# Kernel optimization log

Measured on AMD Instinct MI355X. Metric: run time of the kernel, lower is better.

The kernel has to match this reference:

```python
import jax, jax.numpy as jnp
import numpy as np

N, NS, D, HID = 8192, 512, 1024, 1024  # nodes, num_edges, f_dim, mlp hidden (max(f_dim,128))


def layernorm(x, g, b, eps=1e-5):
    m = x.mean(-1, keepdims=True)
    v = x.var(-1, keepdims=True)
    return (x - m) / jnp.sqrt(v + eps) * g + b


def mask_topk(a, kk):
    # keep only the top-kk entries of each row (vectorized version of mask_attn)
    _, idx = jax.lax.top_k(a, kk)
    rows = jnp.arange(a.shape[0])[:, None]
    mask = jnp.zeros(a.shape, a.dtype).at[rows, idx].set(1.0)
    return a * mask


def setup_inputs() -> dict:
    key = jax.random.key(0)
    ks = jax.random.split(key, 16)
    xavier = lambda k, i, o: jax.random.uniform(k, (i, o), jnp.float32, -1.0, 1.0) * np.sqrt(6.0 / (i + o))
    return {
        "inputs": jax.random.normal(ks[0], (N, D), jnp.float32),
        "noise": jax.random.normal(ks[1], (NS, D), jnp.float32),
        "edges_mu": jax.random.normal(ks[2], (1, D), jnp.float32),
        "edges_logsigma": xavier(ks[3], 1, D),
        "Wq": xavier(ks[4], D, D), "bq": jnp.zeros((D,), jnp.float32),
        "Wk": xavier(ks[5], D, D), "bk": jnp.zeros((D,), jnp.float32),
        "Wv": xavier(ks[6], D, D), "bv": jnp.zeros((D,), jnp.float32),
        "W1": xavier(ks[7], 2 * D, HID), "b1": jnp.zeros((HID,), jnp.float32),
        "W2": xavier(ks[8], HID, D), "b2": jnp.zeros((D,), jnp.float32),
        "g_in": jnp.ones((D,), jnp.float32), "b_in": jnp.zeros((D,), jnp.float32),
        "g_e": jnp.ones((D,), jnp.float32), "b_e": jnp.zeros((D,), jnp.float32),
        "k_n": 64,
        "k_e": 8,
    }


def reference(inputs, noise, edges_mu, edges_logsigma, Wq, bq, Wk, bk, Wv, bv,
              W1, b1, W2, b2, g_in, b_in, g_e, b_e, k_n, k_e):
    n, d = inputs.shape
    scale = d ** -0.5
    eps = 1e-8
    x = layernorm(inputs, g_in, b_in)                       # norm_input
    k = jax.nn.relu(x @ Wk + bk)                            # [N, D]
    v = jax.nn.relu(x @ Wv + bv)                            # [N, D]
    edges = edges_mu + jnp.exp(edges_logsigma) * noise      # [NS, D]
    # single iteration (iters=1)
    edges = layernorm(edges, g_e, b_e)                      # norm_edgs
    q = jax.nn.relu(edges @ Wq + bq)                        # [NS, D]
    dots = jnp.einsum('ni,mi->nm', q, k) * scale            # [NS, N]
    attn = jax.nn.softmax(dots, axis=1) + eps
    attn = attn / attn.sum(axis=1, keepdims=True)
    attn = mask_topk(attn, k_n)
    updates = jnp.einsum('nm,md->nd', attn, v)              # [NS, D]
    edges = jnp.concatenate([edges, updates], axis=1)       # [NS, 2D]
    edges = jax.nn.relu(edges @ W1 + b1) @ W2 + b2          # mlp -> [NS, D]
    q2 = x @ Wq + bq                                        # no relu in source
    k2 = jax.nn.relu(edges @ Wk + bk)                       # [NS, D]
    dots_v = jnp.einsum('ni,mi->nm', q2, k2) * scale        # [N, NS]
    attn_v = jax.nn.softmax(dots_v, axis=1)
    H = mask_topk(attn_v, k_e)
    return edges, H, dots
```

## Files before the change

kernel.cpp:

```cpp
#include <hip/hip_runtime.h>
#include <stdint.h>
#include <stddef.h>

typedef unsigned short u16;
typedef __bf16 bf16x8 __attribute__((ext_vector_type(8)));
typedef float f32x4 __attribute__((ext_vector_type(4)));

#define DEV __device__ __forceinline__

DEV float bf2f(u16 u){ union{uint32_t i; float f;} c; c.i=(uint32_t)u<<16; return c.f; }
DEV u16 f2bf(float f){ union{float f; uint32_t i;} c; c.f=f; uint32_t x=c.i;
  uint32_t r = x + 0x7FFFu + ((x>>16)&1u); return (u16)(r>>16); }
DEV uint32_t fmap(float f){ union{float f; uint32_t u;} c; c.f=f;
  return (c.u & 0x80000000u) ? ~c.u : (c.u | 0x80000000u); }
DEV float funmap(uint32_t u){ union{uint32_t u; float f;} c;
  c.u = (u & 0x80000000u) ? (u & 0x7FFFFFFFu) : ~u; return c.f; }
DEV void split2(float x, u16& h, u16& l){ h = f2bf(x); l = f2bf(x - bf2f(h)); }

DEV float bredsum(float v, float* buf, int tid){
  #pragma unroll
  for(int o=32;o;o>>=1) v += __shfl_down(v,o);
  __syncthreads();
  if((tid&63)==0) buf[tid>>6]=v;
  __syncthreads();
  return buf[0]+buf[1]+buf[2]+buf[3];
}
DEV float bredmax(float v, float* buf, int tid){
  #pragma unroll
  for(int o=32;o;o>>=1) v = fmaxf(v, __shfl_down(v,o));
  __syncthreads();
  if((tid&63)==0) buf[tid>>6]=v;
  __syncthreads();
  return fmaxf(fmaxf(buf[0],buf[1]),fmaxf(buf[2],buf[3]));
}
DEV int bredsumi(int v, int* buf, int tid){
  #pragma unroll
  for(int o=32;o;o>>=1) v += __shfl_down(v,o);
  __syncthreads();
  if((tid&63)==0) buf[tid>>6]=v;
  __syncthreads();
  return buf[0]+buf[1]+buf[2]+buf[3];
}

template<bool RELU, int SK>
__global__ __launch_bounds__(256)
void gemm1_64(const u16* __restrict__ A, int lda,
              const u16* __restrict__ Bt, int ldb,
              const float* __restrict__ bias, float scale,
              u16* __restrict__ outb, float* __restrict__ outf,
              float* __restrict__ part,
              int K, int ldc, int M)
{
  __shared__ __align__(16) u16 As[64*32];
  __shared__ __align__(16) u16 Bs[128*32];
  const int tid = threadIdx.x, lane = tid&63, wave = tid>>6;
  const int m0 = blockIdx.y*64, n0 = blockIdx.x*128;
  const int wm = (wave>>1)*32, wn = (wave&1)*64;
  const int ml = lane&15, quad = lane>>4;
  const int ks = K / SK;
  const int kbeg = blockIdx.z * ks;
  const u16* pa  = A  + (size_t)(m0+(tid>>2))*lda + kbeg + (tid&3)*8;
  const u16* pb0 = Bt + (size_t)(n0+(tid>>2))*ldb + kbeg + (tid&3)*8;
  const u16* pb1 = Bt + (size_t)(n0+64+(tid>>2))*ldb + kbeg + (tid&3)*8;

  f32x4 acc[2][4];
  #pragma unroll
  for(int i=0;i<2;i++)
    #pragma unroll
    for(int j=0;j<4;j++) acc[i][j] = (f32x4){0.f,0.f,0.f,0.f};

  uint4 ra=*(const uint4*)pa, rb0=*(const uint4*)pb0, rb1=*(const uint4*)pb1;
  for(int k0=0;k0<ks;k0+=32){
    __syncthreads();
    *(uint4*)&As[tid*8]       = ra;
    *(uint4*)&Bs[tid*8]       = rb0;
    *(uint4*)&Bs[(256+tid)*8] = rb1;
    __syncthreads();
    if(k0+32<ks){
      ra  = *(const uint4*)(pa +k0+32);
      rb0 = *(const uint4*)(pb0+k0+32);
      rb1 = *(const uint4*)(pb1+k0+32);
    }
    bf16x8 af[2], bf[4];
    #pragma unroll
    for(int mi=0;mi<2;mi++) af[mi] = *(const bf16x8*)&As[(wm+mi*16+ml)*32 + quad*8];
    #pragma unroll
    for(int ni=0;ni<4;ni++) bf[ni] = *(const bf16x8*)&Bs[(wn+ni*16+ml)*32 + quad*8];
    #pragma unroll
    for(int mi=0;mi<2;mi++)
      #pragma unroll
      for(int ni=0;ni<4;ni++)
        acc[mi][ni] = __builtin_amdgcn_mfma_f32_16x16x32_bf16(af[mi], bf[ni], acc[mi][ni], 0,0,0);
  }
  #pragma unroll
  for(int mi=0;mi<2;mi++){
    const int rbase = m0 + wm + mi*16 + quad*4;
    #pragma unroll
    for(int ni=0;ni<4;ni++){
      const int col = n0 + wn + ni*16 + ml;
      if(SK==1){
        const float bv = bias ? bias[col] : 0.f;
        #pragma unroll
        for(int r=0;r<4;r++){
          float v = acc[mi][ni][r]*scale + bv;
          if(RELU) v = fmaxf(v, 0.f);
          const size_t idx = (size_t)(rbase + r)*ldc + col;
          if(outb) outb[idx] = f2bf(v);
          if(outf) outf[idx] = v;
        }
      }else{
        #pragma unroll
        for(int r=0;r<4;r++)
          part[((size_t)blockIdx.z*M + rbase + r)*ldc + col] = acc[mi][ni][r];
      }
    }
  }
}

template<bool RELU, int SK>
__global__ __launch_bounds__(256)
void gemm3_64(const u16* __restrict__ Ah, const u16* __restrict__ Al, int lda,
              const u16* __restrict__ Bh, const u16* __restrict__ Bl, int ldb,
              const float* __restrict__ bias, float scale,
              u16* __restrict__ outh, u16* __restrict__ outl,
              float* __restrict__ outf, float* __restrict__ part,
              int K, int ldc, int M)
{
  __shared__ __align__(16) u16 AsH[64*32];
  __shared__ __align__(16) u16 AsL[64*32];
  __shared__ __align__(16) u16 BsH[128*32];
  __shared__ __align__(16) u16 BsL[128*32];
  const int tid = threadIdx.x, lane = tid&63, wave = tid>>6;
  const int m0 = blockIdx.y*64, n0 = blockIdx.x*128;
  const int wm = (wave>>1)*32, wn = (wave&1)*64;
  const int ml = lane&15, quad = lane>>4;
  const int ks = K / SK;
  const int kbeg = blockIdx.z * ks;
  const size_t ao  = (size_t)(m0+(tid>>2))*lda + kbeg + (tid&3)*8;
  const size_t bo0 = (size_t)(n0+(tid>>2))*ldb + kbeg + (tid&3)*8;
  const size_t bo1 = (size_t)(n0+64+(tid>>2))*ldb + kbeg + (tid&3)*8;

  f32x4 acc[2][4];
  #pragma unroll
  for(int i=0;i<2;i++)
    #pragma unroll
    for(int j=0;j<4;j++) acc[i][j] = (f32x4){0.f,0.f,0.f,0.f};

  uint4 rah=*(const uint4*)(Ah+ao),  ral=*(const uint4*)(Al+ao);
  uint4 rbh0=*(const uint4*)(Bh+bo0), rbl0=*(const uint4*)(Bl+bo0);
  uint4 rbh1=*(const uint4*)(Bh+bo1), rbl1=*(const uint4*)(Bl+bo1);
  for(int k0=0;k0<ks;k0+=32){
    __syncthreads();
    *(uint4*)&AsH[tid*8]       = rah;
    *(uint4*)&AsL[tid*8]       = ral;
    *(uint4*)&BsH[tid*8]       = rbh0;
    *(uint4*)&BsL[tid*8]       = rbl0;
    *(uint4*)&BsH[(256+tid)*8] = rbh1;
    *(uint4*)&BsL[(256+tid)*8] = rbl1;
    __syncthreads();
    if(k0+32<ks){
      const int s = k0+32;
      rah =*(const uint4*)(Ah+ao +s); ral =*(const uint4*)(Al+ao +s);
      rbh0=*(const uint4*)(Bh+bo0+s); rbl0=*(const uint4*)(Bl+bo0+s);
      rbh1=*(const uint4*)(Bh+bo1+s); rbl1=*(const uint4*)(Bl+bo1+s);
    }
    bf16x8 afh[2], afl[2], bfh[4], bfl[4];
    #pragma unroll
    for(int mi=0;mi<2;mi++){
      const int o = (wm+mi*16+ml)*32 + quad*8;
      afh[mi] = *(const bf16x8*)&AsH[o];
      afl[mi] = *(const bf16x8*)&AsL[o];
    }
    #pragma unroll
    for(int ni=0;ni<4;ni++){
      const int o = (wn+ni*16+ml)*32 + quad*8;
      bfh[ni] = *(const bf16x8*)&BsH[o];
      bfl[ni] = *(const bf16x8*)&BsL[o];
    }
    #pragma unroll
    for(int mi=0;mi<2;mi++)
      #pragma unroll
      for(int ni=0;ni<4;ni++){
        acc[mi][ni] = __builtin_amdgcn_mfma_f32_16x16x32_bf16(afh[mi], bfh[ni], acc[mi][ni], 0,0,0);
        acc[mi][ni] = __builtin_amdgcn_mfma_f32_16x16x32_bf16(afh[mi], bfl[ni], acc[mi][ni], 0,0,0);
        acc[mi][ni] = __builtin_amdgcn_mfma_f32_16x16x32_bf16(afl[mi], bfh[ni], acc[mi][ni], 0,0,0);
      }
  }
  #pragma unroll
  for(int mi=0;mi<2;mi++){
    const int rbase = m0 + wm + mi*16 + quad*4;
    #pragma unroll
    for(int ni=0;ni<4;ni++){
      const int col = n0 + wn + ni*16 + ml;
      if(SK==1){
        const float bv = bias ? bias[col] : 0.f;
        #pragma unroll
        for(int r=0;r<4;r++){
          float v = acc[mi][ni][r]*scale + bv;
          if(RELU) v = fmaxf(v, 0.f);
          const size_t idx = (size_t)(rbase + r)*ldc + col;
          if(outh){ u16 h, l; split2(v, h, l); outh[idx] = h; outl[idx] = l; }
          if(outf) outf[idx] = v;
        }
      }else{
        #pragma unroll
        for(int r=0;r<4;r++)
          part[((size_t)blockIdx.z*M + rbase + r)*ldc + col] = acc[mi][ni][r];
      }
    }
  }
}

template<bool RELU, int SK>
__global__ __launch_bounds__(256)
void reduce_epi(const float* __restrict__ part, const float* __restrict__ bias,
                float scale, u16* __restrict__ outh, u16* __restrict__ outl,
                u16* __restrict__ outb, float* __restrict__ outf,
                size_t MN, int N)
{
  const size_t i = ((size_t)blockIdx.x*256 + threadIdx.x)*4;
  float4 s = *(const float4*)(part + i);
  #pragma unroll
  for(int z=1; z<SK; z++){
    const float4 t = *(const float4*)(part + (size_t)z*MN + i);
    s.x += t.x; s.y += t.y; s.z += t.z; s.w += t.w;
  }
  const int col = (int)(i % (size_t)N);
  float4 bv = bias ? *(const float4*)(bias + col) : (float4){0.f,0.f,0.f,0.f};
  float v[4] = { s.x*scale + bv.x, s.y*scale + bv.y, s.z*scale + bv.z, s.w*scale + bv.w };
  if(RELU){
    #pragma unroll
    for(int j=0;j<4;j++) v[j] = fmaxf(v[j], 0.f);
  }
  if(outh){
    ushort4 h4, l4;
    split2(v[0], h4.x, l4.x); split2(v[1], h4.y, l4.y);
    split2(v[2], h4.z, l4.z); split2(v[3], h4.w, l4.w);
    *(ushort4*)(outh + i) = h4;
    *(ushort4*)(outl + i) = l4;
  }
  if(outb){
    ushort4 b4;
    b4.x=f2bf(v[0]); b4.y=f2bf(v[1]); b4.z=f2bf(v[2]); b4.w=f2bf(v[3]);
    *(ushort4*)(outb + i) = b4;
  }
  if(outf) *(float4*)(outf + i) = (float4){v[0],v[1],v[2],v[3]};
}

__global__ __launch_bounds__(256)
void transpose_split(const float* __restrict__ in, u16* __restrict__ outh,
                     u16* __restrict__ outl, int R, int C)
{
  __shared__ float tile[32][33];
  const int tx = threadIdx.x & 31, ty = threadIdx.x >> 5;
  const int bx = blockIdx.x*32, by = blockIdx.y*32;
  #pragma unroll
  for(int i=0;i<32;i+=8)
    tile[ty+i][tx] = in[(size_t)(by+ty+i)*C + bx + tx];
  __syncthreads();
  #pragma unroll
  for(int i=0;i<32;i+=8){
    const float v = tile[tx][ty+i];
    u16 h, l; split2(v, h, l);
    const size_t o = (size_t)(bx+ty+i)*R + by + tx;
    outh[o] = h; outl[o] = l;
  }
}
__global__ __launch_bounds__(256)
void transpose_plain(const float* __restrict__ in, u16* __restrict__ outh, int R, int C)
{
  __shared__ float tile[32][33];
  const int tx = threadIdx.x & 31, ty = threadIdx.x >> 5;
  const int bx = blockIdx.x*32, by = blockIdx.y*32;
  #pragma unroll
  for(int i=0;i<32;i+=8)
    tile[ty+i][tx] = in[(size_t)(by+ty+i)*C + bx + tx];
  __syncthreads();
  #pragma unroll
  for(int i=0;i<32;i+=8)
    outh[(size_t)(bx+ty+i)*R + by + tx] = f2bf(tile[tx][ty+i]);
}
__global__ __launch_bounds__(256)
void split_convert(const float* __restrict__ in, u16* __restrict__ oh,
                   u16* __restrict__ ol)
{
  const int i = blockIdx.x*256 + threadIdx.x;
  const float4 v = ((const float4*)in)[i];
  ushort4 h4, l4;
  split2(v.x, h4.x, l4.x); split2(v.y, h4.y, l4.y);
  split2(v.z, h4.z, l4.z); split2(v.w, h4.w, l4.w);
  ((ushort4*)oh)[i] = h4; ((ushort4*)ol)[i] = l4;
}

__global__ __launch_bounds__(256)
void layernorm_rows(const float* __restrict__ in, const float* __restrict__ g,
                    const float* __restrict__ bb, u16* __restrict__ outh,
                    u16* __restrict__ outl, int ostride)
{
  __shared__ float buf[4];
  const int row = blockIdx.x, tid = threadIdx.x;
  const float4 xv = ((const float4*)(in + (size_t)row*1024))[tid];
  float s  = bredsum(xv.x+xv.y+xv.z+xv.w, buf, tid);
  float s2 = bredsum(xv.x*xv.x+xv.y*xv.y+xv.z*xv.z+xv.w*xv.w, buf, tid);
  const float mean = s * (1.f/1024.f);
  const float var  = s2 * (1.f/1024.f) - mean*mean;
  const float rs   = 1.f / sqrtf(var + 1e-5f);
  const float4 gv = ((const float4*)g)[tid];
  const float4 bv = ((const float4*)bb)[tid];
  float o0 = (xv.x-mean)*rs*gv.x + bv.x;
  float o1 = (xv.y-mean)*rs*gv.y + bv.y;
  float o2 = (xv.z-mean)*rs*gv.z + bv.z;
  float o3 = (xv.w-mean)*rs*gv.w + bv.w;
  ushort4 oh, ol;
  split2(o0, oh.x, ol.x); split2(o1, oh.y, ol.y);
  split2(o2, oh.z, ol.z); split2(o3, oh.w, ol.w);
  ((ushort4*)(outh + (size_t)row*ostride))[tid] = oh;
  ((ushort4*)(outl + (size_t)row*ostride))[tid] = ol;
}

__global__ __launch_bounds__(256)
void edges_ln(const float* __restrict__ noise, const float* __restrict__ mu,
              const float* __restrict__ lsig, const float* __restrict__ g,
              const float* __restrict__ bb, u16* __restrict__ outh,
              u16* __restrict__ outl, int ostride)
{
  __shared__ float buf[4];
  const int row = blockIdx.x, tid = threadIdx.x;
  const float4 nv  = ((const float4*)(noise + (size_t)row*1024))[tid];
  const float4 muv = ((const float4*)mu)[tid];
  const float4 lsv = ((const float4*)lsig)[tid];
  float v0 = muv.x + expf(lsv.x)*nv.x;
  float v1 = muv.y + expf(lsv.y)*nv.y;
  float v2 = muv.z + expf(lsv.z)*nv.z;
  float v3 = muv.w + expf(lsv.w)*nv.w;
  float s  = bredsum(v0+v1+v2+v3, buf, tid);
  float s2 = bredsum(v0*v0+v1*v1+v2*v2+v3*v3, buf, tid);
  const float mean = s * (1.f/1024.f);
  const float var  = s2 * (1.f/1024.f) - mean*mean;
  const float rs   = 1.f / sqrtf(var + 1e-5f);
  const float4 gv = ((const float4*)g)[tid];
  const float4 bv = ((const float4*)bb)[tid];
  float o0 = (v0-mean)*rs*gv.x + bv.x;
  float o1 = (v1-mean)*rs*gv.y + bv.y;
  float o2 = (v2-mean)*rs*gv.z + bv.z;
  float o3 = (v3-mean)*rs*gv.w + bv.w;
  ushort4 oh, ol;
  split2(o0, oh.x, ol.x); split2(o1, oh.y, ol.y);
  split2(o2, oh.z, ol.z); split2(o3, oh.w, ol.w);
  ((ushort4*)(outh + (size_t)row*ostride))[tid] = oh;
  ((ushort4*)(outl + (size_t)row*ostride))[tid] = ol;
}

#define USI(i) ((i) + ((i)>>5))
__global__ __launch_bounds__(256)
void softmax_topk_a(const float* __restrict__ dots, const int* __restrict__ knp,
                    int* __restrict__ tidx, float* __restrict__ tw)
{
  const int NC = 8192;
  __shared__ uint32_t us[8192 + 256];
  __shared__ float fbuf[4];
  __shared__ int ibuf[4];
  __shared__ int scan[256];
  __shared__ int slot_ctr;
  const int row = blockIdx.x, tid = threadIdx.x;
  const float* x = dots + (size_t)row * NC;

  float mx = -3.4e38f;
  for(int i=tid;i<NC;i+=256){ float f = x[i]; us[USI(i)] = fmap(f); mx = fmaxf(mx, f); }
  mx = bredmax(mx, fbuf, tid);
  float se = 0.f;
  for(int i=tid;i<NC;i+=256) se += expf(funmap(us[USI(i)]) - mx);
  se = bredsum(se, fbuf, tid);
  float ts = 0.f;
  for(int i=tid;i<NC;i+=256) ts += expf(funmap(us[USI(i)]) - mx)/se + 1e-8f;
  const float T = bredsum(ts, fbuf, tid);

  const int k = knp[0];
  uint32_t lo = 0u, hi = 0xFFFFFFFFu;
  const int base = tid*32;
  while(lo < hi){
    const uint32_t mid = lo + ((hi - lo) >> 1) + 1u;
    int c = 0;
    #pragma unroll 8
    for(int j=0;j<32;j++) c += (us[USI(base+j)] >= mid);
    c = bredsumi(c, ibuf, tid);
    if(c >= k) lo = mid; else hi = mid - 1u;
  }
  const uint32_t uth = lo;
  int gt = 0, eq = 0;
  #pragma unroll 8
  for(int j=0;j<32;j++){ uint32_t u = us[USI(base+j)]; gt += (u>uth); eq += (u==uth); }
  const int c1 = bredsumi(gt, ibuf, tid);
  __syncthreads();
  scan[tid] = eq;
  __syncthreads();
  #pragma unroll
  for(int o=1;o<256;o<<=1){
    int t = (tid>=o) ? scan[tid-o] : 0;
    __syncthreads();
    scan[tid] += t;
    __syncthreads();
  }
  int eq_rank = scan[tid] - eq;
  const int budget = k - c1;
  if(tid==0) slot_ctr = 0;
  __syncthreads();
  for(int j=0;j<32;j++){
    const int i = base + j;
    const uint32_t u = us[USI(i)];
    bool sel = (u > uth);
    if(u == uth){ sel = (eq_rank < budget); eq_rank++; }
    if(sel){
      const int s = atomicAdd(&slot_ctr, 1);
      const float f = funmap(u);
      const float w = (expf(f - mx)/se + 1e-8f) / T;
      if(s < 128){ tidx[row*128 + s] = i; tw[row*128 + s] = w; }
    }
  }
}

__global__ __launch_bounds__(256)
void gather_updates(const int* __restrict__ tidx, const float* __restrict__ tw,
                    const int* __restrict__ knp, const u16* __restrict__ v,
                    u16* __restrict__ cath, u16* __restrict__ catl)
{
  __shared__ int   idx_s[128];
  __shared__ float w_s[128];
  const int row = blockIdx.x, tid = threadIdx.x;
  const int kk = knp[0];
  if(tid < 128){
    idx_s[tid] = (tid < kk) ? (tidx[row*128+tid] & 8191) : 0;
    w_s[tid]   = (tid < kk) ? tw[row*128+tid] : 0.f;
  }
  __syncthreads();
  const int c = tid*4;
  float a0=0,a1=0,a2=0,a3=0;
  for(int j=0;j<kk && j<128;j++){
    const ushort4 vv = *(const ushort4*)&v[(size_t)idx_s[j]*1024 + c];
    const float w = w_s[j];
    a0 += w*bf2f(vv.x); a1 += w*bf2f(vv.y); a2 += w*bf2f(vv.z); a3 += w*bf2f(vv.w);
  }
  ushort4 oh, ol;
  split2(a0, oh.x, ol.x); split2(a1, oh.y, ol.y);
  split2(a2, oh.z, ol.z); split2(a3, oh.w, ol.w);
  ((ushort4*)(cath + (size_t)row*2048 + 1024))[tid] = oh;
  ((ushort4*)(catl + (size_t)row*2048 + 1024))[tid] = ol;
}

__global__ __launch_bounds__(256)
void bias_v_kernel(const float* __restrict__ bq, const u16* __restrict__ k2h,
                   const u16* __restrict__ k2l, float* __restrict__ out)
{
  __shared__ float buf[4];
  const int row = blockIdx.x, tid = threadIdx.x;
  const ushort4 h4 = ((const ushort4*)(k2h + (size_t)row*1024))[tid];
  const ushort4 l4 = ((const ushort4*)(k2l + (size_t)row*1024))[tid];
  const float4 b4 = ((const float4*)bq)[tid];
  float s = b4.x*(bf2f(h4.x)+bf2f(l4.x)) + b4.y*(bf2f(h4.y)+bf2f(l4.y))
          + b4.z*(bf2f(h4.z)+bf2f(l4.z)) + b4.w*(bf2f(h4.w)+bf2f(l4.w));
  s = bredsum(s, buf, tid);
  if(tid==0) out[row] = s * 0.03125f;
}

__global__ __launch_bounds__(256)
void softmax_topk_h_wave(const float* __restrict__ dv, const int* __restrict__ kep,
                         float* __restrict__ H)
{
  const int wave = threadIdx.x >> 6, lane = threadIdx.x & 63;
  const int row = blockIdx.x*4 + wave;
  const float* x = dv + (size_t)row*512 + lane*8;
  const float4 a = *(const float4*)x;
  const float4 b = *(const float4*)(x+4);
  float vals[8] = {a.x,a.y,a.z,a.w,b.x,b.y,b.z,b.w};

  float mx = vals[0];
  #pragma unroll
  for(int j=1;j<8;j++) mx = fmaxf(mx, vals[j]);
  #pragma unroll
  for(int o=32;o;o>>=1) mx = fmaxf(mx, __shfl_xor(mx, o));
  float e[8], se = 0.f;
  #pragma unroll
  for(int j=0;j<8;j++){ e[j] = expf(vals[j]-mx); se += e[j]; }
  #pragma unroll
  for(int o=32;o;o>>=1) se += __shfl_xor(se, o);
  const float inv = 1.f/se;

  const int k = kep[0];
  unsigned int selmask = 0;
  for(int r=0;r<k;r++){
    unsigned long long best = 0;
    #pragma unroll
    for(int j=0;j<8;j++){
      if(!((selmask>>j)&1u)){
        const unsigned long long key =
          ((unsigned long long)fmap(vals[j]) << 9) | (unsigned long long)(511 - (lane*8+j));
        if(key > best) best = key;
      }
    }
    #pragma unroll
    for(int o=32;o;o>>=1){
      const unsigned long long other = __shfl_xor(best, o);
      if(other > best) best = other;
    }
    const int bidx = 511 - (int)(best & 511ull);
    if((bidx>>3) == lane) selmask |= 1u << (bidx & 7);
  }

  float4 o0, o1;
  o0.x = (selmask&  1u) ? e[0]*inv : 0.f;
  o0.y = (selmask&  2u) ? e[1]*inv : 0.f;
  o0.z = (selmask&  4u) ? e[2]*inv : 0.f;
  o0.w = (selmask&  8u) ? e[3]*inv : 0.f;
  o1.x = (selmask& 16u) ? e[4]*inv : 0.f;
  o1.y = (selmask& 32u) ? e[5]*inv : 0.f;
  o1.z = (selmask& 64u) ? e[6]*inv : 0.f;
  o1.w = (selmask&128u) ? e[7]*inv : 0.f;
  float* outp = H + (size_t)row*512 + lane*8;
  *(float4*)outp     = o0;
  *(float4*)(outp+4) = o1;
}

extern "C" void kernel_launch(void* const* d_in, const int* in_sizes, int n_in,
                              void* d_out, int out_size, void* d_ws, size_t ws_size,
                              hipStream_t stream)
{
  const float* inputs = (const float*)d_in[0];
  const float* noise  = (const float*)d_in[1];
  const float* emu    = (const float*)d_in[2];
  const float* elsig  = (const float*)d_in[3];
  const float* Wq = (const float*)d_in[4];  const float* bq = (const float*)d_in[5];
  const float* Wk = (const float*)d_in[6];  const float* bk = (const float*)d_in[7];
  const float* Wv = (const float*)d_in[8];  const float* bv = (const float*)d_in[9];
  const float* W1 = (const float*)d_in[10]; const float* b1 = (const float*)d_in[11];
  const float* W2 = (const float*)d_in[12]; const float* b2 = (const float*)d_in[13];
  const float* g_in = (const float*)d_in[14]; const float* b_in = (const float*)d_in[15];
  const float* g_e  = (const float*)d_in[16]; const float* b_e  = (const float*)d_in[17];
  const int* knp = (const int*)d_in[18];
  const int* kep = (const int*)d_in[19];

  float* out = (float*)d_out;
  float* out_edges = out;
  float* out_H     = out + 512*1024;
  float* out_dots  = out + 512*1024 + 8192*512;

  char* p = (char*)d_ws;
  const size_t MB = 1024ull*1024;
  u16* xh = (u16*)(p + 0*MB);
  u16* xl = (u16*)(p + 16*MB);
  u16* kb = (u16*)(p + 32*MB);
  u16* vb = (u16*)(p + 48*MB);
  float* dotsvf = (float*)(p + 32*MB);
  u16* WkTh = (u16*)(p + 64*MB);  u16* WkTl = (u16*)(p + 66*MB);
  u16* WvTh = (u16*)(p + 68*MB);
  u16* WqTh = (u16*)(p + 70*MB);
  u16* Wqh  = (u16*)(p + 72*MB);  u16* Wql  = (u16*)(p + 74*MB);
  u16* W1Th = (u16*)(p + 76*MB);  u16* W1Tl = (u16*)(p + 80*MB);
  u16* W2Th = (u16*)(p + 84*MB);  u16* W2Tl = (u16*)(p + 86*MB);
  u16* cath = (u16*)(p + 88*MB);  u16* catl = (u16*)(p + 90*MB);
  u16* qmb  = (u16*)(p + 92*MB);
  u16* h1h  = (u16*)(p + 93*MB);  u16* h1l  = (u16*)(p + 94*MB);
  u16* eoh  = (u16*)(p + 95*MB);  u16* eol  = (u16*)(p + 96*MB);
  u16* k2h  = (u16*)(p + 97*MB);  u16* k2l  = (u16*)(p + 98*MB);
  u16* Gth  = (u16*)(p + 99*MB);  u16* Gtl  = (u16*)(p + 100*MB);
  int*   tidx  = (int*)  (p + 101*MB);
  float* tw    = (float*)(p + 101*MB + 256*1024);
  float* biasv = (float*)(p + 101*MB + 512*1024);
  float* part  = (float*)(p + 104*MB);

  hipMemsetAsync(tidx, 0, 512ull*128*4, stream);
  hipMemsetAsync(tw,   0, 512ull*128*4, stream);

  transpose_split<<<dim3(32,32),256,0,stream>>>(Wk, WkTh, WkTl, 1024, 1024);
  transpose_split<<<dim3(32,64),256,0,stream>>>(W1, W1Th, W1Tl, 2048, 1024);
  transpose_split<<<dim3(32,32),256,0,stream>>>(W2, W2Th, W2Tl, 1024, 1024);
  transpose_plain<<<dim3(32,32),256,0,stream>>>(Wv, WvTh, 1024, 1024);
  transpose_plain<<<dim3(32,32),256,0,stream>>>(Wq, WqTh, 1024, 1024);
  split_convert<<<1024,256,0,stream>>>(Wq, Wqh, Wql);

  layernorm_rows<<<8192,256,0,stream>>>(inputs, g_in, b_in, xh, xl, 1024);
  edges_ln<<<512,256,0,stream>>>(noise, emu, elsig, g_e, b_e, cath, catl, 2048);

  const size_t MN = 512ull*1024;
  gemm1_64<true,1><<<dim3(8,128),256,0,stream>>>(xh,1024, WkTh,1024, bk, 1.f,
                                                 kb,nullptr, nullptr, 1024,1024,8192);
  gemm1_64<true,1><<<dim3(8,128),256,0,stream>>>(xh,1024, WvTh,1024, bv, 1.f,
                                                 vb,nullptr, nullptr, 1024,1024,8192);
  gemm1_64<false,4><<<dim3(8,8,4),256,0,stream>>>(cath,2048, WqTh,1024, nullptr, 1.f,
                                                  nullptr,nullptr, part, 1024,1024,512);
  reduce_epi<true,4><<<512,256,0,stream>>>(part, bq, 1.f, nullptr,nullptr, qmb,nullptr, MN, 1024);
  gemm1_64<false,1><<<dim3(64,8),256,0,stream>>>(qmb,1024, kb,1024, nullptr, 0.03125f,
                                                 nullptr,out_dots, nullptr, 1024,8192,512);
  softmax_topk_a<<<512,256,0,stream>>>(out_dots, knp, tidx, tw);
  gather_updates<<<512,256,0,stream>>>(tidx, tw, knp, vb, cath, catl);

  gemm3_64<false,4><<<dim3(8,8,4),256,0,stream>>>(cath,catl,2048, W1Th,W1Tl,2048,
                                                  nullptr,1.f, nullptr,nullptr,nullptr,
                                                  part, 2048,1024,512);
  reduce_epi<true,4><<<512,256,0,stream>>>(part, b1, 1.f, h1h,h1l, nullptr,nullptr, MN, 1024);
  gemm3_64<false,4><<<dim3(8,8,4),256,0,stream>>>(h1h,h1l,1024, W2Th,W2Tl,1024,
                                                  nullptr,1.f, nullptr,nullptr,nullptr,
                                                  part, 1024,1024,512);
  reduce_epi<false,4><<<512,256,0,stream>>>(part, b2, 1.f, eoh,eol, nullptr,out_edges, MN, 1024);
  gemm3_64<false,4><<<dim3(8,8,4),256,0,stream>>>(eoh,eol,1024, WkTh,WkTl,1024,
                                                  nullptr,1.f, nullptr,nullptr,nullptr,
                                                  part, 1024,1024,512);
  reduce_epi<true,4><<<512,256,0,stream>>>(part, bk, 1.f, k2h,k2l, nullptr,nullptr, MN, 1024);
  gemm3_64<false,4><<<dim3(8,8,4),256,0,stream>>>(k2h,k2l,1024, Wqh,Wql,1024,
                                                  nullptr,1.f, nullptr,nullptr,nullptr,
                                                  part, 1024,1024,512);
  reduce_epi<false,4><<<512,256,0,stream>>>(part, nullptr, 1.f, Gth,Gtl, nullptr,nullptr, MN, 1024);
  bias_v_kernel<<<512,256,0,stream>>>(bq, k2h, k2l, biasv);
  gemm3_64<false,1><<<dim3(4,128),256,0,stream>>>(xh,xl,1024, Gth,Gtl,1024,
                                                  biasv, 0.03125f, nullptr,nullptr,dotsvf,
                                                  nullptr, 1024,512,8192);
  softmax_topk_h_wave<<<2048,256,0,stream>>>(dotsvf, kep, out_H);
}
```

Before: 429.5 us.

## Replace bitwise binary-search top-k with radix histogram select in softmax kernel

The per-row top-k threshold search changes from a 32-step binary search, each step needing a block reduction, to a 4-pass 8-bit radix select. Each pass builds a shared-memory histogram with atomics and scans it in one wave. The kernel also loads rows as float4 into an XOR-swizzled shared buffer instead of a padded one. The second softmax normalisation sum is replaced by the closed form 1 + N*eps. That closed form drops one full exp pass but assumes the softmax sums to exactly one, and the shared atomics can contend when many values share a bucket.

```diff
diff --git a/kernel.cpp b/kernel.cpp
--- a/kernel.cpp
+++ b/kernel.cpp
@@ -351,45 +351,103 @@
   ((ushort4*)(outl + (size_t)row*ostride))[tid] = ol;
 }
 
-#define USI(i) ((i) + ((i)>>5))
+#define SWZ(i) ((i) ^ (((((unsigned)(i))>>5)&7u)<<2))
 __global__ __launch_bounds__(256)
 void softmax_topk_a(const float* __restrict__ dots, const int* __restrict__ knp,
                     int* __restrict__ tidx, float* __restrict__ tw)
 {
   const int NC = 8192;
-  __shared__ uint32_t us[8192 + 256];
+  __shared__ __align__(16) uint32_t us[8192];
   __shared__ float fbuf[4];
   __shared__ int ibuf[4];
   __shared__ int scan[256];
+  __shared__ uint32_t hist[256];
+  __shared__ uint32_t bcast;
   __shared__ int slot_ctr;
   const int row = blockIdx.x, tid = threadIdx.x;
+  const int lane = tid & 63, wave = tid >> 6;
   const float* x = dots + (size_t)row * NC;
 
   float mx = -3.4e38f;
-  for(int i=tid;i<NC;i+=256){ float f = x[i]; us[USI(i)] = fmap(f); mx = fmaxf(mx, f); }
+  #pragma unroll
+  for(int it=0; it<8; ++it){
+    const int i = (tid + it*256)*4;
+    const float4 f = *(const float4*)(x + i);
+    mx = fmaxf(fmaxf(mx, fmaxf(f.x,f.y)), fmaxf(f.z,f.w));
+    uint4 u; u.x=fmap(f.x); u.y=fmap(f.y); u.z=fmap(f.z); u.w=fmap(f.w);
+    *(uint4*)&us[SWZ(i)] = u;
+  }
   mx = bredmax(mx, fbuf, tid);
+
   float se = 0.f;
-  for(int i=tid;i<NC;i+=256) se += expf(funmap(us[USI(i)]) - mx);
+  #pragma unroll
+  for(int it=0; it<8; ++it){
+    const int i = (tid + it*256)*4;
+    const uint4 u = *(const uint4*)&us[SWZ(i)];
+    se += expf(funmap(u.x)-mx) + expf(funmap(u.y)-mx)
+        + expf(funmap(u.z)-mx) + expf(funmap(u.w)-mx);
+  }
   se = bredsum(se, fbuf, tid);
-  float ts = 0.f;
-  for(int i=tid;i<NC;i+=256) ts += expf(funmap(us[USI(i)]) - mx)/se + 1e-8f;
-  const float T = bredsum(ts, fbuf, tid);
+  const float T = 1.f + (float)NC * 1e-8f;
 
   const int k = knp[0];
-  uint32_t lo = 0u, hi = 0xFFFFFFFFu;
   const int base = tid*32;
-  while(lo < hi){
-    const uint32_t mid = lo + ((hi - lo) >> 1) + 1u;
-    int c = 0;
-    #pragma unroll 8
-    for(int j=0;j<32;j++) c += (us[USI(base+j)] >= mid);
-    c = bredsumi(c, ibuf, tid);
-    if(c >= k) lo = mid; else hi = mid - 1u;
-  }
-  const uint32_t uth = lo;
+
+  uint32_t prefix = 0;
+  int remaining = k;
+  #pragma unroll
+  for(int shift=24; shift>=0; shift-=8){
+    hist[tid] = 0;
+    __syncthreads();
+    const uint32_t himask = (shift==24) ? 0u : (0xFFFFFFFFu << (shift+8));
+    #pragma unroll
+    for(int j=0;j<32;j+=4){
+      const uint4 u4 = *(const uint4*)&us[SWZ(base+j)];
+      const uint32_t uu[4] = {u4.x,u4.y,u4.z,u4.w};
+      #pragma unroll
+      for(int t=0;t<4;t++)
+        if((uu[t] & himask) == prefix) atomicAdd(&hist[(uu[t]>>shift)&255u], 1u);
+    }
+    __syncthreads();
+    if(wave==0){
+      const uint32_t h0=hist[4*lane], h1=hist[4*lane+1],
+                     h2=hist[4*lane+2], h3=hist[4*lane+3];
+      const uint32_t s3=h3, s2=h2+s3, s1=h1+s2, s0=h0+s1;
+      uint32_t tsum = s0;
+      #pragma unroll
+      for(int o=1;o<64;o<<=1){
+        const uint32_t vv = __shfl_down(tsum, o);
+        if(lane + o < 64) tsum += vv;
+      }
+      const uint32_t excl = tsum - s0;
+      const uint32_t r = (uint32_t)remaining;
+      int cand = -1; uint32_t gsel = 0;
+      if     (s3+excl >= r){ cand = 4*lane+3; gsel = excl; }
+      else if(s2+excl >= r){ cand = 4*lane+2; gsel = s3+excl; }
+      else if(s1+excl >= r){ cand = 4*lane+1; gsel = s2+excl; }
+      else if(s0+excl >= r){ cand = 4*lane+0; gsel = s1+excl; }
+      int bestc = cand; uint32_t bestg = gsel;
+      #pragma unroll
+      for(int o=32;o;o>>=1){
+        const int oc = __shfl_xor(bestc, o);
+        const uint32_t og = __shfl_xor(bestg, o);
+        if(oc > bestc){ bestc = oc; bestg = og; }
+      }
+      if(lane==0) bcast = (uint32_t)bestc;
+      remaining -= (int)bestg;
+    }
+    __syncthreads();
+    prefix |= bcast << shift;
+  }
+  const uint32_t uth = prefix;
+
   int gt = 0, eq = 0;
-  #pragma unroll 8
-  for(int j=0;j<32;j++){ uint32_t u = us[USI(base+j)]; gt += (u>uth); eq += (u==uth); }
+  #pragma unroll
+  for(int j=0;j<32;j+=4){
+    const uint4 u4 = *(const uint4*)&us[SWZ(base+j)];
+    gt += (u4.x>uth)+(u4.y>uth)+(u4.z>uth)+(u4.w>uth);
+    eq += (u4.x==uth)+(u4.y==uth)+(u4.z==uth)+(u4.w==uth);
+  }
   const int c1 = bredsumi(gt, ibuf, tid);
   __syncthreads();
   scan[tid] = eq;
@@ -405,16 +463,21 @@
   const int budget = k - c1;
   if(tid==0) slot_ctr = 0;
   __syncthreads();
-  for(int j=0;j<32;j++){
-    const int i = base + j;
-    const uint32_t u = us[USI(i)];
-    bool sel = (u > uth);
-    if(u == uth){ sel = (eq_rank < budget); eq_rank++; }
-    if(sel){
-      const int s = atomicAdd(&slot_ctr, 1);
-      const float f = funmap(u);
-      const float w = (expf(f - mx)/se + 1e-8f) / T;
-      if(s < 128){ tidx[row*128 + s] = i; tw[row*128 + s] = w; }
+  #pragma unroll 2
+  for(int j=0;j<32;j+=4){
+    const uint4 u4 = *(const uint4*)&us[SWZ(base+j)];
+    const uint32_t uu[4] = {u4.x,u4.y,u4.z,u4.w};
+    #pragma unroll
+    for(int t=0;t<4;t++){
+      const uint32_t u = uu[t];
+      bool sel = (u > uth);
+      if(u == uth){ sel = (eq_rank < budget); eq_rank++; }
+      if(sel){
+        const int s = atomicAdd(&slot_ctr, 1);
+        const float f = funmap(u);
+        const float w = (expf(f - mx)/se + 1e-8f) / T;
+        if(s < 128){ tidx[row*128 + s] = base + j + t; tw[row*128 + s] = w; }
+      }
     }
   }
 }
```

Result: faster. 413.2 us (-3.8%).
